# Kernel tuning notes

Measured on AMD Instinct MI355X. Metric: run time of the kernel, lower is better.

Reference implementation:

```python
import jax, jax.numpy as jnp
import numpy as np

D_MODEL = 2048
NUM_HEADS = 32
HEAD_DIM = D_MODEL // NUM_HEADS  # 64
ROPE_BASE = 10000.0


def _rope_cos_sin(seq_len, head_dim, dtype):
    inv_freq = 1.0 / (ROPE_BASE ** (jnp.arange(0, head_dim, 2, dtype=jnp.float32) / head_dim))
    freqs = jnp.arange(seq_len, dtype=jnp.float32)[:, None] * inv_freq[None, :]  # (S, Dh/2)
    emb = jnp.concatenate([freqs, freqs], axis=-1)  # (S, Dh)
    return emb.astype(dtype), jnp.cos(emb).astype(dtype), jnp.sin(emb).astype(dtype)


def _rotate_half(x):
    x1, x2 = jnp.split(x, 2, axis=-1)
    return jnp.concatenate([-x2, x1], axis=-1)


def setup_inputs() -> dict:
    key = jax.random.key(0)
    k1, k2, k3, k4 = jax.random.split(key, 4)
    B, S, D = 1, 2048, D_MODEL
    x = jax.random.normal(k1, (B, S, D), dtype=jnp.float32)
    Wqkv = jax.random.normal(k2, (3 * D, D), dtype=jnp.float32) * 0.02
    Wo = jax.random.normal(k3, (D, D), dtype=jnp.float32) * 0.02
    gate = jax.random.normal(k4, (D,), dtype=jnp.float32) * 0.1
    return {"x": x, "Wqkv": Wqkv, "Wo": Wo, "gate": gate}


def reference(x, Wqkv, Wo, gate):
    B, S, D = x.shape
    H, Dh = NUM_HEADS, HEAD_DIM
    residual = x

    # fused QKV projection (torch Linear: y = x @ W.T)
    qkv = jnp.einsum('bsd,ed->bse', x, Wqkv).reshape(B, S, 3, H, Dh)
    q, k, v = qkv[:, :, 0], qkv[:, :, 1], qkv[:, :, 2]  # each (B, S, H, Dh)

    # RoPE
    _, cos, sin = _rope_cos_sin(S, Dh, x.dtype)
    cos = cos[None, :, None, :]  # (1, S, 1, Dh)
    sin = sin[None, :, None, :]
    q = q * cos + _rotate_half(q) * sin
    k = k * cos + _rotate_half(k) * sin

    # causal SDPA
    scale = 1.0 / np.sqrt(Dh)
    scores = jnp.einsum('bqhd,bkhd->bhqk', q, k) * scale  # (B, H, S, S)
    causal = jnp.tril(jnp.ones((S, S), dtype=bool))
    scores = jnp.where(causal[None, None], scores, jnp.finfo(scores.dtype).min)
    probs = jax.nn.softmax(scores, axis=-1)
    attn = jnp.einsum('bhqk,bkhd->bqhd', probs, v).reshape(B, S, D)

    out = jnp.einsum('bsd,ed->bse', attn, Wo)
    # HeoGate: learned per-channel gated residual (assumption; see notes)
    return residual + gate * out
```

## Files before the change

### kernel.cpp

```cpp
#include <hip/hip_runtime.h>
#include <hip/hip_bf16.h>
#include <cstdint>
#include <cstddef>

typedef __hip_bfloat16 bf16;
typedef short short8 __attribute__((ext_vector_type(8)));
typedef float f32x4 __attribute__((ext_vector_type(4)));

#define S_LEN 2048
#define DMODEL 2048
#define NQKV 6144
#define NHEADS 32
#define HDIM 64
#define ROPE_L2 0.4152410118609203f
#define Q_PRESCALE 0.18033688011112042f

__device__ __forceinline__ void async_copy16(const bf16* g, bf16* l) {
  __builtin_amdgcn_global_load_lds(
      (const __attribute__((address_space(1))) void*)g,
      (__attribute__((address_space(3))) void*)l, 16, 0, 0);
}

__device__ __forceinline__ f32x4 mfma_bf16(short8 a, short8 b, f32x4 c) {
  return __builtin_amdgcn_mfma_f32_16x16x32_bf16(a, b, c, 0, 0, 0);
}

__global__ __launch_bounds__(256) void cvt3_kernel(const float* __restrict__ sx,
                                                   bf16* __restrict__ dx,
                                                   const float* __restrict__ sw,
                                                   bf16* __restrict__ dw,
                                                   const float* __restrict__ so,
                                                   bf16* __restrict__ dov) {
  int i = blockIdx.x * 256 + threadIdx.x;
  const float* s;
  bf16* d;
  if (i < 1048576) {
    s = sx; d = dx;
  } else if (i < 4194304) {
    s = sw; d = dw; i -= 1048576;
  } else {
    s = so; d = dov; i -= 4194304;
  }
  const float4 v = ((const float4*)s)[i];
  union { bf16 h[4]; ushort4 u; } tmp;
  tmp.h[0] = __float2bfloat16(v.x);
  tmp.h[1] = __float2bfloat16(v.y);
  tmp.h[2] = __float2bfloat16(v.z);
  tmp.h[3] = __float2bfloat16(v.w);
  ((ushort4*)d)[i] = tmp.u;
}

#define QKV_NT 32
#define QBAR() do { __builtin_amdgcn_s_barrier(); __builtin_amdgcn_sched_barrier(0); } while (0)
#define WAITV(n) asm volatile("s_waitcnt vmcnt(" #n ")" ::: "memory")
#define LGKM0() do { asm volatile("s_waitcnt lgkmcnt(0)" ::: "memory"); \
                     __builtin_amdgcn_sched_barrier(0); } while (0)

__global__ __launch_bounds__(256, 2) void gemm_qkv(const bf16* __restrict__ A,
                                                   const bf16* __restrict__ W,
                                                   bf16* __restrict__ q_ws,
                                                   bf16* __restrict__ k_ws,
                                                   bf16* __restrict__ v_ws) {
  __shared__ bf16 smem[32768];
  const int tid = threadIdx.x;
  const int wave = tid >> 6, lane = tid & 63;
  const int wm = wave >> 1, wn = wave & 1;
  const int m0 = blockIdx.y * 128, n0 = blockIdx.x * 128;
  const int srow = tid >> 2;
  const int swc = (((tid & 3) ^ ((tid >> 3) & 3)) * 8);
  const int fr = lane & 15, fq = lane >> 4;
  const int rdc = ((fq ^ ((fr >> 1) & 3)) * 8);

  const bf16* Asrc = A + (size_t)(m0 + srow) * DMODEL + swc;
  const bf16* Bsrc = W + (size_t)(n0 + srow) * DMODEL + swc;

  auto stage = [&](int t_, int bufe_) {
#pragma unroll
    for (int kk = 0; kk < 2; ++kk) {
      const int ko = t_ * 64 + kk * 32;
      async_copy16(Asrc + ko, &smem[bufe_ + kk * 4096 + wave * 512]);
      async_copy16(Asrc + (size_t)64 * DMODEL + ko,
                   &smem[bufe_ + kk * 4096 + 2048 + wave * 512]);
      async_copy16(Bsrc + ko, &smem[bufe_ + 8192 + kk * 4096 + wave * 512]);
      async_copy16(Bsrc + (size_t)64 * DMODEL + ko,
                   &smem[bufe_ + 8192 + kk * 4096 + 2048 + wave * 512]);
    }
  };

  const f32x4 zero = {0.f, 0.f, 0.f, 0.f};
  f32x4 acc[4][4];
#pragma unroll
  for (int i = 0; i < 4; ++i)
#pragma unroll
    for (int j = 0; j < 4; ++j) acc[i][j] = zero;
  short8 a0[4], a1[4], b0[4], b1[4];

  stage(0, 0);
  stage(1, 16384);
  WAITV(8);
  QBAR();

#pragma unroll 2
  for (int t = 0; t < QKV_NT; ++t) {
    const int bc = (t & 1) * 16384;
#pragma unroll
    for (int mi = 0; mi < 4; ++mi) {
      const int ro = (wm * 64 + mi * 16 + fr) * 32 + rdc;
      a0[mi] = *(const short8*)&smem[bc + ro];
      a1[mi] = *(const short8*)&smem[bc + 4096 + ro];
    }
#pragma unroll
    for (int n = 0; n < 4; ++n) {
      const int ro = (wn * 64 + n * 16 + fr) * 32 + rdc;
      b0[n] = *(const short8*)&smem[bc + 8192 + ro];
      b1[n] = *(const short8*)&smem[bc + 12288 + ro];
    }
    LGKM0();
    QBAR();
    if (t + 2 < QKV_NT) stage(t + 2, bc);
    __builtin_amdgcn_s_setprio(1);
#pragma unroll
    for (int mi = 0; mi < 4; ++mi)
#pragma unroll
      for (int n = 0; n < 4; ++n)
        acc[mi][n] = mfma_bf16(a0[mi], b0[n], acc[mi][n]);
#pragma unroll
    for (int mi = 0; mi < 4; ++mi)
#pragma unroll
      for (int n = 0; n < 4; ++n)
        acc[mi][n] = mfma_bf16(a1[mi], b1[n], acc[mi][n]);
    __builtin_amdgcn_s_setprio(0);
    if (t + 2 < QKV_NT)      { WAITV(8); }
    else if (t + 1 < QKV_NT) { WAITV(0); }
    QBAR();
  }

  const int colb = n0 + wn * 64;
  const int sect = colb >> 11;
  const int h = (colb & 2047) >> 6;
  const int col = fr, rq = fq * 4;

  if (sect < 2) {
    bf16* dst = ((sect == 0) ? q_ws : k_ws) + (size_t)h * S_LEN * HDIM;
    bf16* rep = smem + wave * 1152;
    const float qs = (sect == 0) ? Q_PRESCALE : 1.0f;
    const float f0 = exp2f(-(float)col * ROPE_L2);
    const float f1 = exp2f(-(float)(16 + col) * ROPE_L2);
    __syncthreads();
    for (int m = 0; m < 4; ++m) {
      const int base_s = m0 + wm * 64 + m * 16;
#pragma unroll
      for (int jl = 0; jl < 2; ++jl) {
        const int dh = jl * 16 + col;
        const float fr_ = (jl == 0) ? f0 : f1;
#pragma unroll
        for (int r = 0; r < 4; ++r) {
          const int srw = base_s + rq + r;
          float sn, cs;
          __sincosf((float)srw * fr_, &sn, &cs);
          const float xl = acc[m][jl][r], xh = acc[m][jl + 2][r];
          rep[(rq + r) * 72 + dh]      = __float2bfloat16((xl * cs - xh * sn) * qs);
          rep[(rq + r) * 72 + dh + 32] = __float2bfloat16((xh * cs + xl * sn) * qs);
        }
      }
#pragma unroll
      for (int p = 0; p < 2; ++p) {
        const int rr = p * 8 + (lane >> 3), ch = lane & 7;
        const uint4 vv = *(const uint4*)&rep[rr * 72 + ch * 8];
        *(uint4*)&dst[(size_t)(base_s + rr) * HDIM + ch * 8] = vv;
      }
    }
  } else {
    bf16* dst = v_ws + (size_t)h * HDIM * S_LEN;
    for (int j = 0; j < 4; ++j) {
      const int dh = j * 16 + col;
      for (int m = 0; m < 4; ++m) {
        const int s0 = m0 + wm * 64 + m * 16 + rq;
        union { bf16 hx[4]; uint2 u; } vk;
#pragma unroll
        for (int r = 0; r < 4; ++r) vk.hx[r] = __float2bfloat16(acc[m][j][r]);
        *(uint2*)&dst[(size_t)dh * S_LEN + s0] = vk.u;
      }
    }
  }
}

__global__ __launch_bounds__(512) void attn_kernel(const bf16* __restrict__ q_ws,
                                                   const bf16* __restrict__ k_ws,
                                                   const bf16* __restrict__ vt_ws,
                                                   bf16* __restrict__ attn_out) {
  const int bid = blockIdx.x;
  const int pr = bid >> 5;
  const int h = bid & 31;

  const int tid = threadIdx.x, wave = tid >> 6, lane = tid & 63;
  const int col = lane & 15, fq = lane >> 4;

  __shared__ bf16 Ks[2][64 * 64];
  __shared__ bf16 Vs[2][64 * 64];
  __shared__ bf16 Pl[8][16 * 72];
  bf16* pl = Pl[wave];

  const bf16* qh = q_ws + (size_t)h * S_LEN * HDIM;
  const bf16* kh = k_ws + (size_t)h * S_LEN * HDIM;
  const bf16* vh = vt_ws + (size_t)h * HDIM * S_LEN;

  const int srow = lane >> 3;
  const int slot = lane & 7;
  const int schunk = slot ^ srow;

  auto stage = [&](int kt, int buf) {
    const int k0 = kt * 64;
    const int r8 = wave * 8;
    async_copy16(kh + (size_t)(k0 + r8 + srow) * HDIM + schunk * 8,
                 &Ks[buf][r8 * 64]);
    async_copy16(vh + (size_t)(r8 + srow) * S_LEN + k0 + schunk * 8,
                 &Vs[buf][r8 * 64]);
  };

  const f32x4 zero = {0.f, 0.f, 0.f, 0.f};

  for (int pass = 0; pass < 2; ++pass) {
    const int qt = (pass == 0) ? (15 - pr) : pr;
    const int q_glob = qt * 128 + wave * 16 + col;

    short8 qf[2];
#pragma unroll
    for (int ks = 0; ks < 2; ++ks)
      qf[ks] = *(const short8*)&qh[(size_t)q_glob * HDIM + ks * 32 + fq * 8];

    f32x4 o_acc[4] = {zero, zero, zero, zero};
    float m_i = -1e30f, l_i = 0.f;

    stage(0, 0);

    const int lastk = 2 * qt + 1;
    for (int kt = 0; kt <= lastk; ++kt) {
      const int buf = kt & 1;
      const int k0 = kt * 64;
      __syncthreads();
      if (kt < lastk) stage(kt + 1, buf ^ 1);

      short8 kf[8];
#pragma unroll
      for (int n = 0; n < 4; ++n) {
        const int row = n * 16 + col;
#pragma unroll
        for (int ks = 0; ks < 2; ++ks)
          kf[n * 2 + ks] =
              *(const short8*)&Ks[buf][row * 64 + (((ks * 4 + fq) ^ (row & 7)) * 8)];
      }
      f32x4 s_acc[4] = {zero, zero, zero, zero};
#pragma unroll
      for (int n = 0; n < 4; ++n)
#pragma unroll
        for (int ks = 0; ks < 2; ++ks)
          s_acc[n] = mfma_bf16(kf[n * 2 + ks], qf[ks], s_acc[n]);

      short8 vf[8];
#pragma unroll
      for (int n = 0; n < 4; ++n) {
        const int row = n * 16 + col;
#pragma unroll
        for (int ks = 0; ks < 2; ++ks)
          vf[n * 2 + ks] =
              *(const short8*)&Vs[buf][row * 64 + (((ks * 4 + fq) ^ (row & 7)) * 8)];
      }

      if (k0 + 63 > qt * 128 + wave * 16) {
#pragma unroll
        for (int n = 0; n < 4; ++n)
#pragma unroll
          for (int r = 0; r < 4; ++r)
            if (k0 + n * 16 + fq * 4 + r > q_glob) s_acc[n][r] = -1e30f;
      }

      float vmax = -1e30f;
#pragma unroll
      for (int n = 0; n < 4; ++n)
#pragma unroll
        for (int r = 0; r < 4; ++r) vmax = fmaxf(vmax, s_acc[n][r]);
      vmax = fmaxf(vmax, __shfl_xor(vmax, 16, 64));
      vmax = fmaxf(vmax, __shfl_xor(vmax, 32, 64));

      if (!__all(vmax - m_i <= 8.0f)) {
        const float mnew = fmaxf(m_i, vmax);
        const float alpha = exp2f(m_i - mnew);
        l_i *= alpha;
#pragma unroll
        for (int n = 0; n < 4; ++n)
#pragma unroll
          for (int r = 0; r < 4; ++r) o_acc[n][r] *= alpha;
        m_i = mnew;
      }

      float rs = 0.f;
#pragma unroll
      for (int n = 0; n < 4; ++n)
#pragma unroll
        for (int r = 0; r < 4; ++r) {
          const float p = exp2f(s_acc[n][r] - m_i);
          s_acc[n][r] = p;
          rs += p;
        }
      rs += __shfl_xor(rs, 16, 64);
      rs += __shfl_xor(rs, 32, 64);
      l_i += rs;

#pragma unroll
      for (int n = 0; n < 4; ++n) {
        union { bf16 hx[4]; uint2 u; } pk;
#pragma unroll
        for (int r = 0; r < 4; ++r) pk.hx[r] = __float2bfloat16(s_acc[n][r]);
        *(uint2*)&pl[col * 72 + n * 16 + fq * 4] = pk.u;
      }
      short8 pa[2];
#pragma unroll
      for (int ks = 0; ks < 2; ++ks)
        pa[ks] = *(const short8*)&pl[col * 72 + ks * 32 + fq * 8];

#pragma unroll
      for (int n = 0; n < 4; ++n)
#pragma unroll
        for (int ks = 0; ks < 2; ++ks)
          o_acc[n] = mfma_bf16(vf[n * 2 + ks], pa[ks], o_acc[n]);
    }

    const float inv = 1.0f / l_i;
#pragma unroll
    for (int n = 0; n < 4; ++n) {
#pragma unroll
      for (int r = 0; r < 4; ++r) o_acc[n][r] *= inv;
      union { bf16 hx[4]; uint2 u; } ok;
#pragma unroll
      for (int r = 0; r < 4; ++r) ok.hx[r] = __float2bfloat16(o_acc[n][r]);
      *(uint2*)&attn_out[(size_t)q_glob * DMODEL + h * HDIM + n * 16 + fq * 4] = ok.u;
    }
  }
}

__global__ __launch_bounds__(256) void gemm_out(const bf16* __restrict__ A,
                                                const bf16* __restrict__ W,
                                                const float* __restrict__ xres,
                                                const float* __restrict__ gate,
                                                float* __restrict__ out) {
  constexpr int K = DMODEL;
  constexpr int NT = K / 32;
  __shared__ bf16 As[3][64 * 32];
  __shared__ bf16 Bs[3][128 * 32];
  const int tid = threadIdx.x;
  const int wave = tid >> 6, lane = tid & 63;
  const int m0 = blockIdx.y * 64, n0 = blockIdx.x * 128;
  const int sr = lane >> 2;
  const int swc = (((lane & 3) ^ ((lane >> 3) & 3)) * 8);
  const int fr = lane & 15, fq = lane >> 4;
  const int rdc = ((fq ^ ((fr >> 1) & 3)) * 8);

  auto stage = [&](int t_, int s_) {
    async_copy16(A + (size_t)(m0 + wave * 16 + sr) * K + t_ * 32 + swc,
                 &As[s_][(wave * 16) * 32]);
#pragma unroll
    for (int j = 0; j < 2; ++j)
      async_copy16(W + (size_t)(n0 + wave * 32 + j * 16 + sr) * K + t_ * 32 + swc,
                   &Bs[s_][(wave * 32 + j * 16) * 32]);
  };

  const f32x4 zero = {0.f, 0.f, 0.f, 0.f};
  f32x4 acc[4][2];
  for (int i = 0; i < 4; ++i)
    for (int j = 0; j < 2; ++j) acc[i][j] = zero;

  stage(0, 0);
  stage(1, 1);
  WAITV(3);
  QBAR();

  for (int t = 0; t < NT; ++t) {
    const int s = t % 3;
    short8 a[4], b[2];
#pragma unroll
    for (int i = 0; i < 4; ++i)
      a[i] = *(const short8*)&As[s][(i * 16 + fr) * 32 + rdc];
#pragma unroll
    for (int j = 0; j < 2; ++j)
      b[j] = *(const short8*)&Bs[s][(wave * 32 + j * 16 + fr) * 32 + rdc];
    LGKM0();
    QBAR();
    if (t + 2 < NT) stage(t + 2, (t + 2) % 3);
#pragma unroll
    for (int i = 0; i < 4; ++i)
#pragma unroll
      for (int j = 0; j < 2; ++j)
        acc[i][j] = mfma_bf16(a[i], b[j], acc[i][j]);
    if (t + 1 < NT) {
      if (t + 2 < NT) { WAITV(3); }
      else            { WAITV(0); }
      QBAR();
    }
  }

  const int col = fr, rq = fq * 4;
  for (int j = 0; j < 2; ++j) {
    const int cc = n0 + wave * 32 + j * 16 + col;
    const float g = gate[cc];
    for (int i = 0; i < 4; ++i) {
      const int base_row = m0 + i * 16 + rq;
      for (int r = 0; r < 4; ++r) {
        const size_t idx = (size_t)(base_row + r) * DMODEL + cc;
        out[idx] = xres[idx] + g * acc[i][j][r];
      }
    }
  }
}

extern "C" void kernel_launch(void* const* d_in, const int* in_sizes, int n_in,
                              void* d_out, int out_size, void* d_ws, size_t ws_size,
                              hipStream_t stream) {
  const float* x    = (const float*)d_in[0];
  const float* Wqkv = (const float*)d_in[1];
  const float* Wo   = (const float*)d_in[2];
  const float* gate = (const float*)d_in[3];
  float* out = (float*)d_out;

  char* ws = (char*)d_ws;
  const size_t MB = 1024 * 1024;
  bf16* xb      = (bf16*)(ws);
  bf16* wqkvb   = (bf16*)(ws + 8 * MB);
  bf16* wob     = (bf16*)(ws + 32 * MB);
  bf16* q_ws    = (bf16*)(ws + 40 * MB);
  bf16* k_ws    = (bf16*)(ws + 48 * MB);
  bf16* v_ws    = (bf16*)(ws + 56 * MB);
  bf16* attn_ws = (bf16*)(ws);

  cvt3_kernel<<<dim3(20480), 256, 0, stream>>>(x, xb, Wqkv, wqkvb, Wo, wob);

  gemm_qkv<<<dim3(NQKV / 128, S_LEN / 128), 256, 0, stream>>>(xb, wqkvb, q_ws, k_ws, v_ws);
  attn_kernel<<<dim3(256), 512, 0, stream>>>(q_ws, k_ws, v_ws, attn_ws);
  gemm_out<<<dim3(DMODEL / 128, DMODEL / 64), 256, 0, stream>>>(attn_ws, wob, x, gate, out);
}
```

Before: 253.2 us.

## Split attention into one block per q-tile and deepen gemm_out K-step

The attention kernel used to process two paired q-tiles per block, one after the other, for load balance. It now launches 512 blocks, one per q-tile and head, ordered heaviest first, which doubles grid parallelism but makes per-block work uneven. The output GEMM now steps K by 64 instead of 32, using double-buffered shared memory instead of a triple buffer. It also raises MFMA issue priority with s_setprio and adds an occupancy hint to launch bounds, aiming to cut barrier count and improve overlap.

```diff
diff --git a/kernel.cpp b/kernel.cpp
--- a/kernel.cpp
+++ b/kernel.cpp
@@ -190,11 +190,12 @@
                                                    const bf16* __restrict__ vt_ws,
                                                    bf16* __restrict__ attn_out) {
   const int bid = blockIdx.x;
-  const int pr = bid >> 5;
+  const int qt = 15 - (bid >> 5);
   const int h = bid & 31;
 
   const int tid = threadIdx.x, wave = tid >> 6, lane = tid & 63;
   const int col = lane & 15, fq = lane >> 4;
+  const int q_glob = qt * 128 + wave * 16 + col;
 
   __shared__ bf16 Ks[2][64 * 64];
   __shared__ bf16 Vs[2][64 * 64];
@@ -218,185 +219,196 @@
                  &Vs[buf][r8 * 64]);
   };
 
+  short8 qf[2];
+#pragma unroll
+  for (int ks = 0; ks < 2; ++ks)
+    qf[ks] = *(const short8*)&qh[(size_t)q_glob * HDIM + ks * 32 + fq * 8];
+
   const f32x4 zero = {0.f, 0.f, 0.f, 0.f};
-
-  for (int pass = 0; pass < 2; ++pass) {
-    const int qt = (pass == 0) ? (15 - pr) : pr;
-    const int q_glob = qt * 128 + wave * 16 + col;
-
-    short8 qf[2];
+  f32x4 o_acc[4] = {zero, zero, zero, zero};
+  float m_i = -1e30f, l_i = 0.f;
+
+  stage(0, 0);
+
+  const int lastk = 2 * qt + 1;
+  for (int kt = 0; kt <= lastk; ++kt) {
+    const int buf = kt & 1;
+    const int k0 = kt * 64;
+    __syncthreads();
+    if (kt < lastk) stage(kt + 1, buf ^ 1);
+
+    short8 kf[8];
+#pragma unroll
+    for (int n = 0; n < 4; ++n) {
+      const int row = n * 16 + col;
+#pragma unroll
+      for (int ks = 0; ks < 2; ++ks)
+        kf[n * 2 + ks] =
+            *(const short8*)&Ks[buf][row * 64 + (((ks * 4 + fq) ^ (row & 7)) * 8)];
+    }
+    f32x4 s_acc[4] = {zero, zero, zero, zero};
+#pragma unroll
+    for (int n = 0; n < 4; ++n)
+#pragma unroll
+      for (int ks = 0; ks < 2; ++ks)
+        s_acc[n] = mfma_bf16(kf[n * 2 + ks], qf[ks], s_acc[n]);
+
+    short8 vf[8];
+#pragma unroll
+    for (int n = 0; n < 4; ++n) {
+      const int row = n * 16 + col;
+#pragma unroll
+      for (int ks = 0; ks < 2; ++ks)
+        vf[n * 2 + ks] =
+            *(const short8*)&Vs[buf][row * 64 + (((ks * 4 + fq) ^ (row & 7)) * 8)];
+    }
+
+    if (k0 + 63 > qt * 128 + wave * 16) {
+#pragma unroll
+      for (int n = 0; n < 4; ++n)
+#pragma unroll
+        for (int r = 0; r < 4; ++r)
+          if (k0 + n * 16 + fq * 4 + r > q_glob) s_acc[n][r] = -1e30f;
+    }
+
+    float vmax = -1e30f;
+#pragma unroll
+    for (int n = 0; n < 4; ++n)
+#pragma unroll
+      for (int r = 0; r < 4; ++r) vmax = fmaxf(vmax, s_acc[n][r]);
+    vmax = fmaxf(vmax, __shfl_xor(vmax, 16, 64));
+    vmax = fmaxf(vmax, __shfl_xor(vmax, 32, 64));
+
+    if (!__all(vmax - m_i <= 8.0f)) {
+      const float mnew = fmaxf(m_i, vmax);
+      const float alpha = exp2f(m_i - mnew);
+      l_i *= alpha;
+#pragma unroll
+      for (int n = 0; n < 4; ++n)
+#pragma unroll
+        for (int r = 0; r < 4; ++r) o_acc[n][r] *= alpha;
+      m_i = mnew;
+    }
+
+    float rs = 0.f;
+#pragma unroll
+    for (int n = 0; n < 4; ++n)
+#pragma unroll
+      for (int r = 0; r < 4; ++r) {
+        const float p = exp2f(s_acc[n][r] - m_i);
+        s_acc[n][r] = p;
+        rs += p;
+      }
+    rs += __shfl_xor(rs, 16, 64);
+    rs += __shfl_xor(rs, 32, 64);
+    l_i += rs;
+
+#pragma unroll
+    for (int n = 0; n < 4; ++n) {
+      union { bf16 hx[4]; uint2 u; } pk;
+#pragma unroll
+      for (int r = 0; r < 4; ++r) pk.hx[r] = __float2bfloat16(s_acc[n][r]);
+      *(uint2*)&pl[col * 72 + n * 16 + fq * 4] = pk.u;
+    }
+    short8 pa[2];
 #pragma unroll
     for (int ks = 0; ks < 2; ++ks)
-      qf[ks] = *(const short8*)&qh[(size_t)q_glob * HDIM + ks * 32 + fq * 8];
-
-    f32x4 o_acc[4] = {zero, zero, zero, zero};
-    float m_i = -1e30f, l_i = 0.f;
-
-    stage(0, 0);
-
-    const int lastk = 2 * qt + 1;
-    for (int kt = 0; kt <= lastk; ++kt) {
-      const int buf = kt & 1;
-      const int k0 = kt * 64;
-      __syncthreads();
-      if (kt < lastk) stage(kt + 1, buf ^ 1);
-
-      short8 kf[8];
-#pragma unroll
-      for (int n = 0; n < 4; ++n) {
-        const int row = n * 16 + col;
-#pragma unroll
-        for (int ks = 0; ks < 2; ++ks)
-          kf[n * 2 + ks] =
-              *(const short8*)&Ks[buf][row * 64 + (((ks * 4 + fq) ^ (row & 7)) * 8)];
-      }
-      f32x4 s_acc[4] = {zero, zero, zero, zero};
-#pragma unroll
-      for (int n = 0; n < 4; ++n)
-#pragma unroll
-        for (int ks = 0; ks < 2; ++ks)
-          s_acc[n] = mfma_bf16(kf[n * 2 + ks], qf[ks], s_acc[n]);
-
-      short8 vf[8];
-#pragma unroll
-      for (int n = 0; n < 4; ++n) {
-        const int row = n * 16 + col;
-#pragma unroll
-        for (int ks = 0; ks < 2; ++ks)
-          vf[n * 2 + ks] =
-              *(const short8*)&Vs[buf][row * 64 + (((ks * 4 + fq) ^ (row & 7)) * 8)];
-      }
-
-      if (k0 + 63 > qt * 128 + wave * 16) {
-#pragma unroll
-        for (int n = 0; n < 4; ++n)
-#pragma unroll
-          for (int r = 0; r < 4; ++r)
-            if (k0 + n * 16 + fq * 4 + r > q_glob) s_acc[n][r] = -1e30f;
-      }
-
-      float vmax = -1e30f;
-#pragma unroll
-      for (int n = 0; n < 4; ++n)
-#pragma unroll
-        for (int r = 0; r < 4; ++r) vmax = fmaxf(vmax, s_acc[n][r]);
-      vmax = fmaxf(vmax, __shfl_xor(vmax, 16, 64));
-      vmax = fmaxf(vmax, __shfl_xor(vmax, 32, 64));
-
-      if (!__all(vmax - m_i <= 8.0f)) {
-        const float mnew = fmaxf(m_i, vmax);
-        const float alpha = exp2f(m_i - mnew);
-        l_i *= alpha;
-#pragma unroll
-        for (int n = 0; n < 4; ++n)
-#pragma unroll
-          for (int r = 0; r < 4; ++r) o_acc[n][r] *= alpha;
-        m_i = mnew;
-      }
-
-      float rs = 0.f;
-#pragma unroll
-      for (int n = 0; n < 4; ++n)
-#pragma unroll
-        for (int r = 0; r < 4; ++r) {
-          const float p = exp2f(s_acc[n][r] - m_i);
-          s_acc[n][r] = p;
-          rs += p;
-        }
-      rs += __shfl_xor(rs, 16, 64);
-      rs += __shfl_xor(rs, 32, 64);
-      l_i += rs;
-
-#pragma unroll
-      for (int n = 0; n < 4; ++n) {
-        union { bf16 hx[4]; uint2 u; } pk;
-#pragma unroll
-        for (int r = 0; r < 4; ++r) pk.hx[r] = __float2bfloat16(s_acc[n][r]);
-        *(uint2*)&pl[col * 72 + n * 16 + fq * 4] = pk.u;
-      }
-      short8 pa[2];
+      pa[ks] = *(const short8*)&pl[col * 72 + ks * 32 + fq * 8];
+
+#pragma unroll
+    for (int n = 0; n < 4; ++n)
 #pragma unroll
       for (int ks = 0; ks < 2; ++ks)
-        pa[ks] = *(const short8*)&pl[col * 72 + ks * 32 + fq * 8];
-
-#pragma unroll
-      for (int n = 0; n < 4; ++n)
-#pragma unroll
-        for (int ks = 0; ks < 2; ++ks)
-          o_acc[n] = mfma_bf16(vf[n * 2 + ks], pa[ks], o_acc[n]);
-    }
-
-    const float inv = 1.0f / l_i;
-#pragma unroll
-    for (int n = 0; n < 4; ++n) {
-#pragma unroll
-      for (int r = 0; r < 4; ++r) o_acc[n][r] *= inv;
-      union { bf16 hx[4]; uint2 u; } ok;
-#pragma unroll
-      for (int r = 0; r < 4; ++r) ok.hx[r] = __float2bfloat16(o_acc[n][r]);
-      *(uint2*)&attn_out[(size_t)q_glob * DMODEL + h * HDIM + n * 16 + fq * 4] = ok.u;
-    }
-  }
-}
-
-__global__ __launch_bounds__(256) void gemm_out(const bf16* __restrict__ A,
-                                                const bf16* __restrict__ W,
-                                                const float* __restrict__ xres,
-                                                const float* __restrict__ gate,
-                                                float* __restrict__ out) {
+        o_acc[n] = mfma_bf16(vf[n * 2 + ks], pa[ks], o_acc[n]);
+  }
+
+  const float inv = 1.0f / l_i;
+#pragma unroll
+  for (int n = 0; n < 4; ++n) {
+#pragma unroll
+    for (int r = 0; r < 4; ++r) o_acc[n][r] *= inv;
+    union { bf16 hx[4]; uint2 u; } ok;
+#pragma unroll
+    for (int r = 0; r < 4; ++r) ok.hx[r] = __float2bfloat16(o_acc[n][r]);
+    *(uint2*)&attn_out[(size_t)q_glob * DMODEL + h * HDIM + n * 16 + fq * 4] = ok.u;
+  }
+}
+
+__global__ __launch_bounds__(256, 2) void gemm_out(const bf16* __restrict__ A,
+                                                   const bf16* __restrict__ W,
+                                                   const float* __restrict__ xres,
+                                                   const float* __restrict__ gate,
+                                                   float* __restrict__ out) {
   constexpr int K = DMODEL;
-  constexpr int NT = K / 32;
-  __shared__ bf16 As[3][64 * 32];
-  __shared__ bf16 Bs[3][128 * 32];
+  constexpr int NT = K / 64;
+  __shared__ bf16 smem[2][12288];
   const int tid = threadIdx.x;
   const int wave = tid >> 6, lane = tid & 63;
   const int m0 = blockIdx.y * 64, n0 = blockIdx.x * 128;
-  const int sr = lane >> 2;
-  const int swc = (((lane & 3) ^ ((lane >> 3) & 3)) * 8);
+  const int srow = tid >> 2;
+  const int swc = (((tid & 3) ^ ((tid >> 3) & 3)) * 8);
   const int fr = lane & 15, fq = lane >> 4;
   const int rdc = ((fq ^ ((fr >> 1) & 3)) * 8);
 
-  auto stage = [&](int t_, int s_) {
-    async_copy16(A + (size_t)(m0 + wave * 16 + sr) * K + t_ * 32 + swc,
-                 &As[s_][(wave * 16) * 32]);
-#pragma unroll
-    for (int j = 0; j < 2; ++j)
-      async_copy16(W + (size_t)(n0 + wave * 32 + j * 16 + sr) * K + t_ * 32 + swc,
-                   &Bs[s_][(wave * 32 + j * 16) * 32]);
+  const bf16* Asrc = A + (size_t)(m0 + srow) * K + swc;
+  const bf16* Bsrc = W + (size_t)(n0 + srow) * K + swc;
+
+  auto stage = [&](int t_, int buf_) {
+#pragma unroll
+    for (int kk = 0; kk < 2; ++kk) {
+      const int ko = t_ * 64 + kk * 32;
+      async_copy16(Asrc + ko, &smem[buf_][kk * 2048 + wave * 512]);
+      async_copy16(Bsrc + ko, &smem[buf_][4096 + kk * 4096 + wave * 512]);
+      async_copy16(Bsrc + (size_t)64 * K + ko,
+                   &smem[buf_][4096 + kk * 4096 + 2048 + wave * 512]);
+    }
   };
 
   const f32x4 zero = {0.f, 0.f, 0.f, 0.f};
   f32x4 acc[4][2];
+#pragma unroll
   for (int i = 0; i < 4; ++i)
+#pragma unroll
     for (int j = 0; j < 2; ++j) acc[i][j] = zero;
+  short8 a0[4], a1[4], b0[2], b1[2];
 
   stage(0, 0);
   stage(1, 1);
-  WAITV(3);
+  WAITV(6);
   QBAR();
 
   for (int t = 0; t < NT; ++t) {
-    const int s = t % 3;
-    short8 a[4], b[2];
-#pragma unroll
-    for (int i = 0; i < 4; ++i)
-      a[i] = *(const short8*)&As[s][(i * 16 + fr) * 32 + rdc];
-#pragma unroll
-    for (int j = 0; j < 2; ++j)
-      b[j] = *(const short8*)&Bs[s][(wave * 32 + j * 16 + fr) * 32 + rdc];
+    const int bc = t & 1;
+#pragma unroll
+    for (int i = 0; i < 4; ++i) {
+      const int ro = (i * 16 + fr) * 32 + rdc;
+      a0[i] = *(const short8*)&smem[bc][ro];
+      a1[i] = *(const short8*)&smem[bc][2048 + ro];
+    }
+#pragma unroll
+    for (int j = 0; j < 2; ++j) {
+      const int ro = (wave * 32 + j * 16 + fr) * 32 + rdc;
+      b0[j] = *(const short8*)&smem[bc][4096 + ro];
+      b1[j] = *(const short8*)&smem[bc][8192 + ro];
+    }
     LGKM0();
     QBAR();
-    if (t + 2 < NT) stage(t + 2, (t + 2) % 3);
+    if (t + 2 < NT) stage(t + 2, bc);
+    __builtin_amdgcn_s_setprio(1);
 #pragma unroll
     for (int i = 0; i < 4; ++i)
 #pragma unroll
       for (int j = 0; j < 2; ++j)
-        acc[i][j] = mfma_bf16(a[i], b[j], acc[i][j]);
-    if (t + 1 < NT) {
-      if (t + 2 < NT) { WAITV(3); }
-      else            { WAITV(0); }
-      QBAR();
-    }
+        acc[i][j] = mfma_bf16(a0[i], b0[j], acc[i][j]);
+#pragma unroll
+    for (int i = 0; i < 4; ++i)
+#pragma unroll
+      for (int j = 0; j < 2; ++j)
+        acc[i][j] = mfma_bf16(a1[i], b1[j], acc[i][j]);
+    __builtin_amdgcn_s_setprio(0);
+    if (t + 2 < NT)      { WAITV(6); }
+    else if (t + 1 < NT) { WAITV(0); }
+    QBAR();
   }
 
   const int col = fr, rq = fq * 4;
@@ -435,6 +447,6 @@
   cvt3_kernel<<<dim3(20480), 256, 0, stream>>>(x, xb, Wqkv, wqkvb, Wo, wob);
 
   gemm_qkv<<<dim3(NQKV / 128, S_LEN / 128), 256, 0, stream>>>(xb, wqkvb, q_ws, k_ws, v_ws);
-  attn_kernel<<<dim3(256), 512, 0, stream>>>(q_ws, k_ws, v_ws, attn_ws);
+  attn_kernel<<<dim3(512), 512, 0, stream>>>(q_ws, k_ws, v_ws, attn_ws);
   gemm_out<<<dim3(DMODEL / 128, DMODEL / 64), 256, 0, stream>>>(attn_ws, wob, x, gate, out);
 }
```

Measured after the change: 248.2 us. 2.0% less time.
